# Optimization experiments

Measured on AMD Instinct MI355X. Metric: run time of the kernel, lower is better.

## Reference

```python
import jax, jax.numpy as jnp
import numpy as np

N = 100000
E = 1600000
HID = 128
NODE_DIM = 128


def _sage_conv(h, src, dst, W_l, b_l, W_r, n_nodes):
    # PyG SAGEConv (mean aggr): out = lin_l(mean_{j in N(i)} h_j) + lin_r(h_i)
    msg = h[src]                                            # [E, d] gather
    s = jax.ops.segment_sum(msg, dst, num_segments=n_nodes)  # [N, d]
    cnt = jax.ops.segment_sum(jnp.ones((msg.shape[0], 1), h.dtype), dst,
                              num_segments=n_nodes)          # [N, 1]
    agg = jnp.where(cnt > 0, s / jnp.maximum(cnt, 1.0), 0.0)
    return agg @ W_l + b_l + h @ W_r


def setup_inputs() -> dict:
    key = jax.random.key(0)
    ks = jax.random.split(key, 12)
    sc = 0.05
    return {
        "pos": jax.random.normal(ks[0], (N, 3), jnp.float32),
        "atomic_number": jax.random.randint(ks[1], (N,), 0, 10, jnp.int64)
            if jax.config.jax_enable_x64 else jax.random.randint(ks[1], (N,), 0, 10, jnp.int32),
        "edge_index": jax.random.randint(ks[2], (2, E), 0, N, jnp.int32),
        # input_proj: Linear(4, HID) — stored as [in, out]
        "W_in": jax.random.normal(ks[3], (4, HID), jnp.float32) * sc,
        "b_in": jnp.zeros((HID,), jnp.float32),
        # conv1: SAGEConv(HID, HID): lin_l (bias), lin_r (no bias)
        "W1_l": jax.random.normal(ks[4], (HID, HID), jnp.float32) * sc,
        "b1": jnp.zeros((HID,), jnp.float32),
        "W1_r": jax.random.normal(ks[5], (HID, HID), jnp.float32) * sc,
        # conv2
        "W2_l": jax.random.normal(ks[6], (HID, HID), jnp.float32) * sc,
        "b2": jnp.zeros((HID,), jnp.float32),
        "W2_r": jax.random.normal(ks[7], (HID, HID), jnp.float32) * sc,
        # out: Linear(HID, NODE_DIM)
        "W_out": jax.random.normal(ks[8], (HID, NODE_DIM), jnp.float32) * sc,
        "b_out": jnp.zeros((NODE_DIM,), jnp.float32),
    }


def reference(pos, atomic_number, edge_index, W_in, b_in, W1_l, b1, W1_r,
              W2_l, b2, W2_r, W_out, b_out):
    src, dst = edge_index[0], edge_index[1]
    z_atom = (atomic_number.astype(pos.dtype) / 10.0)[:, None]   # [N, 1]
    x = jnp.concatenate([z_atom, pos], axis=-1)                   # [N, 4]
    h = jax.nn.relu(x @ W_in + b_in)
    h = jax.nn.relu(_sage_conv(h, src, dst, W1_l, b1, W1_r, h.shape[0]))
    h = jax.nn.relu(_sage_conv(h, src, dst, W2_l, b2, W2_r, h.shape[0]))
    node_states = h @ W_out + b_out                               # [N, node_dim]
    return node_states.mean(axis=0), node_states
```

## Files before the change

### kernel.cpp

```cpp
#include <hip/hip_runtime.h>

#define HID 128
#define BK_SHIFT 9
#define BK_NODES 512
#define EDGES_PER_BLKA 8192

typedef _Float16 half_t;
typedef __attribute__((ext_vector_type(8))) _Float16 half8;
typedef __attribute__((ext_vector_type(4))) _Float16 half4;
typedef __attribute__((ext_vector_type(2))) _Float16 half2_t;
typedef __attribute__((ext_vector_type(4))) float f32x4;

__global__ __launch_bounds__(256) void k_init(int* __restrict__ bkcnt,
                                              float* __restrict__ outmean) {
  int i = threadIdx.x;
  bkcnt[i] = 0;
  if (i < HID) outmean[i] = 0.f;
}

__global__ __launch_bounds__(256) void k_packW(const float* __restrict__ W,
                                               half_t* __restrict__ out) {
  int tid = blockIdx.x * 256 + threadIdx.x;
  int lane = tid & 63;
  int frag = tid >> 6;
  int ks = frag >> 3, nt = frag & 7;
  int k0 = ks * 32 + ((lane >> 4) << 3);
  int col = nt * 16 + (lane & 15);
  half8 v;
#pragma unroll
  for (int i = 0; i < 8; ++i) v[i] = (half_t)W[(k0 + i) * HID + col];
  *(half8*)&out[(size_t)tid * 8] = v;
}

__global__ __launch_bounds__(256) void k_embed(const float* __restrict__ pos,
                                               const int* __restrict__ an,
                                               const float* __restrict__ Win,
                                               const float* __restrict__ bin,
                                               half_t* __restrict__ h, int n) {
  int t = blockIdx.x * 256 + threadIdx.x;
  int i = t >> 5, cg = t & 31;
  if (i >= n) return;
  int j0 = cg << 2;
  float z  = (float)an[i] / 10.0f;
  float px = pos[3 * i + 0], py = pos[3 * i + 1], pz = pos[3 * i + 2];
  float4 w0 = *(const float4*)&Win[0 * HID + j0];
  float4 w1 = *(const float4*)&Win[1 * HID + j0];
  float4 w2 = *(const float4*)&Win[2 * HID + j0];
  float4 w3 = *(const float4*)&Win[3 * HID + j0];
  float4 b  = *(const float4*)&bin[j0];
  float4 o;
  o.x = fmaxf(fmaf(z, w0.x, fmaf(px, w1.x, fmaf(py, w2.x, fmaf(pz, w3.x, b.x)))), 0.f);
  o.y = fmaxf(fmaf(z, w0.y, fmaf(px, w1.y, fmaf(py, w2.y, fmaf(pz, w3.y, b.y)))), 0.f);
  o.z = fmaxf(fmaf(z, w0.z, fmaf(px, w1.z, fmaf(py, w2.z, fmaf(pz, w3.z, b.z)))), 0.f);
  o.w = fmaxf(fmaf(z, w0.w, fmaf(px, w1.w, fmaf(py, w2.w, fmaf(pz, w3.w, b.w)))), 0.f);
  half4 ph;
  ph.x = (half_t)o.x; ph.y = (half_t)o.y; ph.z = (half_t)o.z; ph.w = (half_t)o.w;
  *(half4*)&h[(size_t)i * HID + j0] = ph;
}

__global__ __launch_bounds__(1024) void k_bhist(const int* __restrict__ dst,
                                                int* __restrict__ bkcnt, int e) {
  __shared__ int hist[256];
  int t = threadIdx.x;
  if (t < 256) hist[t] = 0;
  __syncthreads();
  int e0 = blockIdx.x * EDGES_PER_BLKA;
#pragma unroll
  for (int i = 0; i < 8; ++i) {
    int idx = e0 + i * 1024 + t;
    if (idx < e) atomicAdd(&hist[dst[idx] >> BK_SHIFT], 1);
  }
  __syncthreads();
  if (t < 256 && hist[t] > 0) atomicAdd(&bkcnt[t], hist[t]);
}

__global__ __launch_bounds__(256) void k_bscan(const int* __restrict__ bkcnt,
                                               int* __restrict__ bkbase,
                                               int* __restrict__ bcur,
                                               int nbuck, int e) {
  __shared__ int buf[256];
  int t = threadIdx.x;
  int v = (t < nbuck) ? bkcnt[t] : 0;
  buf[t] = v;
  __syncthreads();
  for (int d = 1; d < 256; d <<= 1) {
    int u = (t >= d) ? buf[t - d] : 0;
    __syncthreads();
    buf[t] += u;
    __syncthreads();
  }
  int excl = buf[t] - v;
  if (t < nbuck) { bkbase[t] = excl; bcur[t] = excl; }
  if (t == 0) bkbase[nbuck] = e;
}

__global__ __launch_bounds__(1024) void k_bucketA(const int* __restrict__ src,
                                                  const int* __restrict__ dst,
                                                  int* __restrict__ bcur,
                                                  unsigned* __restrict__ ebuf,
                                                  int e, int nbuck) {
  __shared__ unsigned stage[EDGES_PER_BLKA];
  __shared__ unsigned char stagebk[EDGES_PER_BLKA];
  __shared__ int hist[256];
  __shared__ int base[256];
  __shared__ int resv[256];
  int t = threadIdx.x;
  if (t < 256) hist[t] = 0;
  __syncthreads();

  int e0 = blockIdx.x * EDGES_PER_BLKA;
  int myb[8], myr[8];
  unsigned mypk[8];
#pragma unroll
  for (int i = 0; i < 8; ++i) {
    int idx = e0 + i * 1024 + t;
    if (idx < e) {
      int d = dst[idx];
      int s = src[idx];
      int b = d >> BK_SHIFT;
      myb[i] = b;
      myr[i] = atomicAdd(&hist[b], 1);
      mypk[i] = ((unsigned)s << BK_SHIFT) | (unsigned)(d & (BK_NODES - 1));
    } else {
      myb[i] = -1;
    }
  }
  __syncthreads();
  if (t < 256) base[t] = hist[t];
  __syncthreads();
  for (int d = 1; d < 256; d <<= 1) {
    int v = 0;
    if (t < 256 && t >= d) v = base[t - d];
    __syncthreads();
    if (t < 256 && t >= d) base[t] += v;
    __syncthreads();
  }
  if (t < 256) {
    base[t] -= hist[t];
    resv[t] = (t < nbuck && hist[t] > 0) ? atomicAdd(&bcur[t], hist[t]) : 0;
  }
  __syncthreads();
#pragma unroll
  for (int i = 0; i < 8; ++i) {
    if (myb[i] >= 0) {
      int slot = base[myb[i]] + myr[i];
      stage[slot] = mypk[i];
      stagebk[slot] = (unsigned char)myb[i];
    }
  }
  __syncthreads();
  int total = e - e0;
  if (total > EDGES_PER_BLKA) total = EDGES_PER_BLKA;
  for (int s = t; s < total; s += 1024) {
    int b = stagebk[s];
    ebuf[resv[b] + (s - base[b])] = stage[s];
  }
}

__global__ __launch_bounds__(256) void k_bucketB(const unsigned* __restrict__ ebuf,
                                                 const int* __restrict__ bkbase,
                                                 int* __restrict__ offs,
                                                 int* __restrict__ csr, int n, int e) {
  __shared__ int hist[BK_NODES];
  __shared__ int pscan[256];
  int b = blockIdx.x;
  int n0 = b << BK_SHIFT;
  int t = threadIdx.x;
  int ebeg = bkbase[b], eend = bkbase[b + 1];
  hist[t] = 0; hist[t + 256] = 0;
  __syncthreads();
  for (int idx = ebeg + t; idx < eend; idx += 256) {
    atomicAdd(&hist[ebuf[idx] & (BK_NODES - 1)], 1);
  }
  __syncthreads();
  int h0 = hist[2 * t], h1 = hist[2 * t + 1];
  int ps = h0 + h1;
  pscan[t] = ps;
  __syncthreads();
  for (int d = 1; d < 256; d <<= 1) {
    int u = (t >= d) ? pscan[t - d] : 0;
    __syncthreads();
    pscan[t] += u;
    __syncthreads();
  }
  int base0 = ebeg + (pscan[t] - ps);
  int g0 = n0 + 2 * t, g1 = g0 + 1;
  if (g0 < n) offs[g0] = base0;
  if (g1 < n) offs[g1] = base0 + h0;
  __syncthreads();
  hist[2 * t] = base0;
  hist[2 * t + 1] = base0 + h0;
  __syncthreads();
  for (int idx = ebeg + t; idx < eend; idx += 256) {
    unsigned pk = ebuf[idx];
    int dl = pk & (BK_NODES - 1);
    int s = (int)(pk >> BK_SHIFT);
    int slot = atomicAdd(&hist[dl], 1);
    csr[slot] = s;
  }
  if (b == 0 && t == 0) offs[n] = e;
}

__global__ __launch_bounds__(256) void k_aggmean_f16(const half_t* __restrict__ h,
                                                     const int* __restrict__ csr,
                                                     const int* __restrict__ offs,
                                                     half_t* __restrict__ out, int n) {
  int w = (blockIdx.x * 256 + threadIdx.x) >> 6;
  int lane = threadIdx.x & 63;
  if (w >= n) return;
  int cs = lane & 15, es = lane >> 4;
  int beg = offs[w], end = offs[w + 1];
  size_t coff = (size_t)(cs * 8);
  float acc[8];
#pragma unroll
  for (int j = 0; j < 8; ++j) acc[j] = 0.f;
  int e = beg;
  for (; e + 16 <= end; e += 16) {
    int s0 = csr[e + es];
    int s1 = csr[e + 4 + es];
    int s2 = csr[e + 8 + es];
    int s3 = csr[e + 12 + es];
    half8 v0 = *(const half8*)&h[(size_t)s0 * HID + coff];
    half8 v1 = *(const half8*)&h[(size_t)s1 * HID + coff];
    half8 v2 = *(const half8*)&h[(size_t)s2 * HID + coff];
    half8 v3 = *(const half8*)&h[(size_t)s3 * HID + coff];
#pragma unroll
    for (int j = 0; j < 8; ++j)
      acc[j] += ((float)v0[j] + (float)v1[j]) + ((float)v2[j] + (float)v3[j]);
  }
  for (; e < end; e += 4) {
    int ee = e + es;
    if (ee < end) {
      int s = csr[ee];
      half8 v = *(const half8*)&h[(size_t)s * HID + coff];
#pragma unroll
      for (int j = 0; j < 8; ++j) acc[j] += (float)v[j];
    }
  }
#pragma unroll
  for (int j = 0; j < 8; ++j) {
    acc[j] += __shfl_xor(acc[j], 16, 64);
    acc[j] += __shfl_xor(acc[j], 32, 64);
  }
  if (es == 0) {
    int c = end - beg;
    float inv = (c > 0) ? 1.0f / (float)c : 0.0f;
    half8 o;
#pragma unroll
    for (int j = 0; j < 8; ++j) o[j] = (half_t)(acc[j] * inv);
    *(half8*)&out[(size_t)w * HID + coff] = o;
  }
}

__global__ __launch_bounds__(256) void k_sage_mfma(const half_t* __restrict__ ha,
                                                   const half_t* __restrict__ hs,
                                                   const half_t* __restrict__ wl,
                                                   const half_t* __restrict__ wr,
                                                   const float* __restrict__ bias,
                                                   half_t* __restrict__ out, int n) {
  int lane = threadIdx.x & 63;
  int wid = threadIdx.x >> 6;
  int row0 = blockIdx.x * 64 + wid * 16;
  if (row0 >= n) return;
  int arow = row0 + (lane & 15);
  int arowc = arow < n ? arow : n - 1;
  size_t abase = (size_t)arowc * HID + ((lane >> 4) << 3);
  const half8* WL = (const half8*)wl;
  const half8* WR = (const half8*)wr;
  f32x4 acc[8];
#pragma unroll
  for (int t = 0; t < 8; ++t) acc[t] = (f32x4){0.f, 0.f, 0.f, 0.f};
#pragma unroll
  for (int ks = 0; ks < 4; ++ks) {
    half8 aD = *(const half8*)&ha[abase + ks * 32];
    half8 aH = *(const half8*)&hs[abase + ks * 32];
    int fb = ks * 8;
#pragma unroll
    for (int nt = 0; nt < 8; ++nt) {
      half8 bl = WL[(size_t)(fb + nt) * 64 + lane];
      half8 br = WR[(size_t)(fb + nt) * 64 + lane];
      acc[nt] = __builtin_amdgcn_mfma_f32_16x16x32_f16(aD, bl, acc[nt], 0, 0, 0);
      acc[nt] = __builtin_amdgcn_mfma_f32_16x16x32_f16(aH, br, acc[nt], 0, 0, 0);
    }
  }
  int rbase = row0 + ((lane >> 4) << 2);
  int cl = lane & 15;
#pragma unroll
  for (int nt = 0; nt < 8; ++nt) {
    int col = nt * 16 + cl;
    float bv = bias[col];
#pragma unroll
    for (int r = 0; r < 4; ++r) {
      int row = rbase + r;
      if (row < n) {
        float v = fmaxf(acc[nt][r] + bv, 0.f);
        out[(size_t)row * HID + col] = (half_t)v;
      }
    }
  }
}

__global__ __launch_bounds__(256) void k_single_mfma(const half_t* __restrict__ hs,
                                                     const half_t* __restrict__ w,
                                                     const float* __restrict__ bias,
                                                     float* __restrict__ out,
                                                     float* __restrict__ part, int n) {
  __shared__ float colsum[HID];
  int tid = threadIdx.x;
  int lane = tid & 63;
  int wid = tid >> 6;
  if (tid < HID) colsum[tid] = 0.f;
  __syncthreads();
  int row0 = blockIdx.x * 64 + wid * 16;
  bool active = row0 < n;
  f32x4 acc[8];
#pragma unroll
  for (int t = 0; t < 8; ++t) acc[t] = (f32x4){0.f, 0.f, 0.f, 0.f};
  if (active) {
    int arow = row0 + (lane & 15);
    int arowc = arow < n ? arow : n - 1;
    size_t abase = (size_t)arowc * HID + ((lane >> 4) << 3);
    const half8* W8 = (const half8*)w;
#pragma unroll
    for (int ks = 0; ks < 4; ++ks) {
      half8 aH = *(const half8*)&hs[abase + ks * 32];
      int fb = ks * 8;
#pragma unroll
      for (int nt = 0; nt < 8; ++nt) {
        half8 b = W8[(size_t)(fb + nt) * 64 + lane];
        acc[nt] = __builtin_amdgcn_mfma_f32_16x16x32_f16(aH, b, acc[nt], 0, 0, 0);
      }
    }
    int rbase = row0 + ((lane >> 4) << 2);
    int cl = lane & 15;
#pragma unroll
    for (int nt = 0; nt < 8; ++nt) {
      int col = nt * 16 + cl;
      float bv = bias[col];
      float csum = 0.f;
#pragma unroll
      for (int r = 0; r < 4; ++r) {
        int row = rbase + r;
        if (row < n) {
          float v = acc[nt][r] + bv;
          out[(size_t)row * HID + col] = v;
          csum += v;
        }
      }
      atomicAdd(&colsum[col], csum);
    }
  }
  __syncthreads();
  if (tid < HID) part[(size_t)blockIdx.x * HID + tid] = colsum[tid];
}

__global__ __launch_bounds__(256) void k_colfinal(const float* __restrict__ part,
                                                  float* __restrict__ outmean,
                                                  int rows, float inv) {
  __shared__ float red[256];
  int t = threadIdx.x;
  int col = t & 127, half = t >> 7;
  int r0 = blockIdx.x * 256;
  float s = 0.f;
  for (int r = half; r < 256; r += 2) {
    int row = r0 + r;
    if (row < rows) s += part[(size_t)row * HID + col];
  }
  red[t] = s;
  __syncthreads();
  if (t < 128) atomicAdd(&outmean[col], (red[t] + red[t + 128]) * inv);
}

extern "C" void kernel_launch(void* const* d_in, const int* in_sizes, int n_in,
                              void* d_out, int out_size, void* d_ws, size_t ws_size,
                              hipStream_t stream) {
  const float* pos  = (const float*)d_in[0];
  const int*   an   = (const int*)d_in[1];
  const int*   ei   = (const int*)d_in[2];
  const float* Win  = (const float*)d_in[3];
  const float* bin  = (const float*)d_in[4];
  const float* W1l  = (const float*)d_in[5];
  const float* b1   = (const float*)d_in[6];
  const float* W1r  = (const float*)d_in[7];
  const float* W2l  = (const float*)d_in[8];
  const float* b2   = (const float*)d_in[9];
  const float* W2r  = (const float*)d_in[10];
  const float* Wout = (const float*)d_in[11];
  const float* bout = (const float*)d_in[12];

  int N = in_sizes[0] / 3;
  int E = in_sizes[2] / 2;
  const int* srcl = ei;
  const int* dstl = ei + E;

  float* outmean = (float*)d_out;
  float* ns      = (float*)d_out + HID;

  char* p = (char*)d_ws;
  auto take = [&](size_t bytes) {
    char* q = p;
    p += (bytes + 255) & ~(size_t)255;
    return q;
  };
  half_t*   H0      = (half_t*)take((size_t)N * HID * 2);
  half_t*   H1      = (half_t*)take((size_t)N * HID * 2);
  half_t*   H2      = (half_t*)take((size_t)N * HID * 2);
  half_t*   D       = (half_t*)take((size_t)N * HID * 2);
  int*      offs    = (int*)take((size_t)(N + 1) * 4);
  int*      csr     = (int*)take((size_t)E * 4);
  unsigned* ebuf    = (unsigned*)take((size_t)E * 4);
  int*      bkcnt   = (int*)take((size_t)256 * 4);
  int*      bkbase  = (int*)take((size_t)257 * 4);
  int*      bcur    = (int*)take((size_t)256 * 4);
  half_t*   pW1l    = (half_t*)take((size_t)16384 * 2);
  half_t*   pW1r    = (half_t*)take((size_t)16384 * 2);
  half_t*   pW2l    = (half_t*)take((size_t)16384 * 2);
  half_t*   pW2r    = (half_t*)take((size_t)16384 * 2);
  half_t*   pWout   = (half_t*)take((size_t)16384 * 2);
  int gSage = (N + 63) / 64;
  float*    colpart = (float*)take((size_t)gSage * HID * 4);

  int nbuck  = (N + BK_NODES - 1) / BK_NODES;
  int gEmbed = (int)(((size_t)N * 32 + 255) / 256);
  int gWave  = (N + 3) / 4;
  int gBktA  = (E + EDGES_PER_BLKA - 1) / EDGES_PER_BLKA;

  k_init<<<1, 256, 0, stream>>>(bkcnt, outmean);
  k_packW<<<8, 256, 0, stream>>>(W1l, pW1l);
  k_packW<<<8, 256, 0, stream>>>(W1r, pW1r);
  k_packW<<<8, 256, 0, stream>>>(W2l, pW2l);
  k_packW<<<8, 256, 0, stream>>>(W2r, pW2r);
  k_packW<<<8, 256, 0, stream>>>(Wout, pWout);
  k_embed<<<gEmbed, 256, 0, stream>>>(pos, an, Win, bin, H0, N);
  k_bhist<<<gBktA, 1024, 0, stream>>>(dstl, bkcnt, E);
  k_bscan<<<1, 256, 0, stream>>>(bkcnt, bkbase, bcur, nbuck, E);
  k_bucketA<<<gBktA, 1024, 0, stream>>>(srcl, dstl, bcur, ebuf, E, nbuck);
  k_bucketB<<<nbuck, 256, 0, stream>>>(ebuf, bkbase, offs, csr, N, E);

  k_aggmean_f16<<<gWave, 256, 0, stream>>>(H0, csr, offs, D, N);
  k_sage_mfma<<<gSage, 256, 0, stream>>>(D, H0, pW1l, pW1r, b1, H1, N);
  k_aggmean_f16<<<gWave, 256, 0, stream>>>(H1, csr, offs, D, N);
  k_sage_mfma<<<gSage, 256, 0, stream>>>(D, H1, pW2l, pW2r, b2, H2, N);
  k_single_mfma<<<gSage, 256, 0, stream>>>(H2, pWout, bout, ns, colpart, N);
  k_colfinal<<<(gSage + 255) / 256, 256, 0, stream>>>(colpart, outmean, gSage, 1.0f / (float)N);
}
```

Before: 320.8 us.

## Use fixed-capacity edge buckets to drop histogram and scan passes

Each destination bucket gets a fixed slot range of BKCAP entries, so the separate bucket-histogram and scan kernels disappear. Bucket cursors are initialised to i*BKCAP, and each node's CSR range now comes from separate begin and end offset arrays. The bucketing kernel also drops its LDS staging and scan, writing edges straight to global memory, and the five weight-packing launches are merged into one. In exchange, global writes are less coalesced, and nothing checks whether a bucket overflows BKCAP, so heavily skewed degree distributions would corrupt memory.

```diff
diff --git a/kernel.cpp b/kernel.cpp
--- a/kernel.cpp
+++ b/kernel.cpp
@@ -3,24 +3,35 @@
 #define HID 128
 #define BK_SHIFT 9
 #define BK_NODES 512
+#define BKCAP 10240
 #define EDGES_PER_BLKA 8192
 
 typedef _Float16 half_t;
 typedef __attribute__((ext_vector_type(8))) _Float16 half8;
 typedef __attribute__((ext_vector_type(4))) _Float16 half4;
-typedef __attribute__((ext_vector_type(2))) _Float16 half2_t;
 typedef __attribute__((ext_vector_type(4))) float f32x4;
 
-__global__ __launch_bounds__(256) void k_init(int* __restrict__ bkcnt,
+__global__ __launch_bounds__(256) void k_init(int* __restrict__ bcur,
                                               float* __restrict__ outmean) {
   int i = threadIdx.x;
-  bkcnt[i] = 0;
+  bcur[i] = i * BKCAP;
   if (i < HID) outmean[i] = 0.f;
 }
 
-__global__ __launch_bounds__(256) void k_packW(const float* __restrict__ W,
-                                               half_t* __restrict__ out) {
-  int tid = blockIdx.x * 256 + threadIdx.x;
+__global__ __launch_bounds__(256) void k_packW5(const float* __restrict__ w0,
+                                                const float* __restrict__ w1,
+                                                const float* __restrict__ w2,
+                                                const float* __restrict__ w3,
+                                                const float* __restrict__ w4,
+                                                half_t* __restrict__ o0,
+                                                half_t* __restrict__ o1,
+                                                half_t* __restrict__ o2,
+                                                half_t* __restrict__ o3,
+                                                half_t* __restrict__ o4) {
+  int m = blockIdx.x >> 3;
+  const float* W = (m == 0) ? w0 : (m == 1) ? w1 : (m == 2) ? w2 : (m == 3) ? w3 : w4;
+  half_t* out = (m == 0) ? o0 : (m == 1) ? o1 : (m == 2) ? o2 : (m == 3) ? o3 : o4;
+  int tid = (blockIdx.x & 7) * 256 + threadIdx.x;
   int lane = tid & 63;
   int frag = tid >> 6;
   int ks = frag >> 3, nt = frag & 7;
@@ -58,56 +69,16 @@
   *(half4*)&h[(size_t)i * HID + j0] = ph;
 }
 
-__global__ __launch_bounds__(1024) void k_bhist(const int* __restrict__ dst,
-                                                int* __restrict__ bkcnt, int e) {
-  __shared__ int hist[256];
-  int t = threadIdx.x;
-  if (t < 256) hist[t] = 0;
-  __syncthreads();
-  int e0 = blockIdx.x * EDGES_PER_BLKA;
-#pragma unroll
-  for (int i = 0; i < 8; ++i) {
-    int idx = e0 + i * 1024 + t;
-    if (idx < e) atomicAdd(&hist[dst[idx] >> BK_SHIFT], 1);
-  }
-  __syncthreads();
-  if (t < 256 && hist[t] > 0) atomicAdd(&bkcnt[t], hist[t]);
-}
-
-__global__ __launch_bounds__(256) void k_bscan(const int* __restrict__ bkcnt,
-                                               int* __restrict__ bkbase,
-                                               int* __restrict__ bcur,
-                                               int nbuck, int e) {
-  __shared__ int buf[256];
-  int t = threadIdx.x;
-  int v = (t < nbuck) ? bkcnt[t] : 0;
-  buf[t] = v;
-  __syncthreads();
-  for (int d = 1; d < 256; d <<= 1) {
-    int u = (t >= d) ? buf[t - d] : 0;
-    __syncthreads();
-    buf[t] += u;
-    __syncthreads();
-  }
-  int excl = buf[t] - v;
-  if (t < nbuck) { bkbase[t] = excl; bcur[t] = excl; }
-  if (t == 0) bkbase[nbuck] = e;
-}
-
 __global__ __launch_bounds__(1024) void k_bucketA(const int* __restrict__ src,
                                                   const int* __restrict__ dst,
                                                   int* __restrict__ bcur,
                                                   unsigned* __restrict__ ebuf,
-                                                  int e, int nbuck) {
-  __shared__ unsigned stage[EDGES_PER_BLKA];
-  __shared__ unsigned char stagebk[EDGES_PER_BLKA];
+                                                  int e) {
   __shared__ int hist[256];
-  __shared__ int base[256];
   __shared__ int resv[256];
   int t = threadIdx.x;
   if (t < 256) hist[t] = 0;
   __syncthreads();
-
   int e0 = blockIdx.x * EDGES_PER_BLKA;
   int myb[8], myr[8];
   unsigned mypk[8];
@@ -126,47 +97,25 @@
     }
   }
   __syncthreads();
-  if (t < 256) base[t] = hist[t];
-  __syncthreads();
-  for (int d = 1; d < 256; d <<= 1) {
-    int v = 0;
-    if (t < 256 && t >= d) v = base[t - d];
-    __syncthreads();
-    if (t < 256 && t >= d) base[t] += v;
-    __syncthreads();
-  }
-  if (t < 256) {
-    base[t] -= hist[t];
-    resv[t] = (t < nbuck && hist[t] > 0) ? atomicAdd(&bcur[t], hist[t]) : 0;
-  }
+  if (t < 256) resv[t] = (hist[t] > 0) ? atomicAdd(&bcur[t], hist[t]) : 0;
   __syncthreads();
 #pragma unroll
   for (int i = 0; i < 8; ++i) {
-    if (myb[i] >= 0) {
-      int slot = base[myb[i]] + myr[i];
-      stage[slot] = mypk[i];
-      stagebk[slot] = (unsigned char)myb[i];
-    }
-  }
-  __syncthreads();
-  int total = e - e0;
-  if (total > EDGES_PER_BLKA) total = EDGES_PER_BLKA;
-  for (int s = t; s < total; s += 1024) {
-    int b = stagebk[s];
-    ebuf[resv[b] + (s - base[b])] = stage[s];
+    if (myb[i] >= 0) ebuf[resv[myb[i]] + myr[i]] = mypk[i];
   }
 }
 
 __global__ __launch_bounds__(256) void k_bucketB(const unsigned* __restrict__ ebuf,
-                                                 const int* __restrict__ bkbase,
+                                                 const int* __restrict__ bkend,
                                                  int* __restrict__ offs,
-                                                 int* __restrict__ csr, int n, int e) {
+                                                 int* __restrict__ offsE,
+                                                 int* __restrict__ csr, int n) {
   __shared__ int hist[BK_NODES];
   __shared__ int pscan[256];
   int b = blockIdx.x;
   int n0 = b << BK_SHIFT;
   int t = threadIdx.x;
-  int ebeg = bkbase[b], eend = bkbase[b + 1];
+  int ebeg = b * BKCAP, eend = bkend[b];
   hist[t] = 0; hist[t + 256] = 0;
   __syncthreads();
   for (int idx = ebeg + t; idx < eend; idx += 256) {
@@ -185,8 +134,8 @@
   }
   int base0 = ebeg + (pscan[t] - ps);
   int g0 = n0 + 2 * t, g1 = g0 + 1;
-  if (g0 < n) offs[g0] = base0;
-  if (g1 < n) offs[g1] = base0 + h0;
+  if (g0 < n) { offs[g0] = base0;      offsE[g0] = base0 + h0; }
+  if (g1 < n) { offs[g1] = base0 + h0; offsE[g1] = base0 + h0 + h1; }
   __syncthreads();
   hist[2 * t] = base0;
   hist[2 * t + 1] = base0 + h0;
@@ -194,22 +143,21 @@
   for (int idx = ebeg + t; idx < eend; idx += 256) {
     unsigned pk = ebuf[idx];
     int dl = pk & (BK_NODES - 1);
-    int s = (int)(pk >> BK_SHIFT);
     int slot = atomicAdd(&hist[dl], 1);
-    csr[slot] = s;
-  }
-  if (b == 0 && t == 0) offs[n] = e;
+    csr[slot] = (int)(pk >> BK_SHIFT);
+  }
 }
 
 __global__ __launch_bounds__(256) void k_aggmean_f16(const half_t* __restrict__ h,
                                                      const int* __restrict__ csr,
                                                      const int* __restrict__ offs,
+                                                     const int* __restrict__ offsE,
                                                      half_t* __restrict__ out, int n) {
   int w = (blockIdx.x * 256 + threadIdx.x) >> 6;
   int lane = threadIdx.x & 63;
   if (w >= n) return;
   int cs = lane & 15, es = lane >> 4;
-  int beg = offs[w], end = offs[w + 1];
+  int beg = offs[w], end = offsE[w];
   size_t coff = (size_t)(cs * 8);
   float acc[8];
 #pragma unroll
@@ -402,15 +350,15 @@
     p += (bytes + 255) & ~(size_t)255;
     return q;
   };
+  int nbuck = (N + BK_NODES - 1) / BK_NODES;
   half_t*   H0      = (half_t*)take((size_t)N * HID * 2);
   half_t*   H1      = (half_t*)take((size_t)N * HID * 2);
   half_t*   H2      = (half_t*)take((size_t)N * HID * 2);
   half_t*   D       = (half_t*)take((size_t)N * HID * 2);
-  int*      offs    = (int*)take((size_t)(N + 1) * 4);
-  int*      csr     = (int*)take((size_t)E * 4);
-  unsigned* ebuf    = (unsigned*)take((size_t)E * 4);
-  int*      bkcnt   = (int*)take((size_t)256 * 4);
-  int*      bkbase  = (int*)take((size_t)257 * 4);
+  int*      offs    = (int*)take((size_t)N * 4);
+  int*      offsE   = (int*)take((size_t)N * 4);
+  int*      csr     = (int*)take((size_t)nbuck * BKCAP * 4);
+  unsigned* ebuf    = (unsigned*)take((size_t)nbuck * BKCAP * 4);
   int*      bcur    = (int*)take((size_t)256 * 4);
   half_t*   pW1l    = (half_t*)take((size_t)16384 * 2);
   half_t*   pW1r    = (half_t*)take((size_t)16384 * 2);
@@ -420,26 +368,20 @@
   int gSage = (N + 63) / 64;
   float*    colpart = (float*)take((size_t)gSage * HID * 4);
 
-  int nbuck  = (N + BK_NODES - 1) / BK_NODES;
   int gEmbed = (int)(((size_t)N * 32 + 255) / 256);
   int gWave  = (N + 3) / 4;
   int gBktA  = (E + EDGES_PER_BLKA - 1) / EDGES_PER_BLKA;
 
-  k_init<<<1, 256, 0, stream>>>(bkcnt, outmean);
-  k_packW<<<8, 256, 0, stream>>>(W1l, pW1l);
-  k_packW<<<8, 256, 0, stream>>>(W1r, pW1r);
-  k_packW<<<8, 256, 0, stream>>>(W2l, pW2l);
-  k_packW<<<8, 256, 0, stream>>>(W2r, pW2r);
-  k_packW<<<8, 256, 0, stream>>>(Wout, pWout);
+  k_init<<<1, 256, 0, stream>>>(bcur, outmean);
+  k_packW5<<<40, 256, 0, stream>>>(W1l, W1r, W2l, W2r, Wout,
+                                   pW1l, pW1r, pW2l, pW2r, pWout);
   k_embed<<<gEmbed, 256, 0, stream>>>(pos, an, Win, bin, H0, N);
-  k_bhist<<<gBktA, 1024, 0, stream>>>(dstl, bkcnt, E);
-  k_bscan<<<1, 256, 0, stream>>>(bkcnt, bkbase, bcur, nbuck, E);
-  k_bucketA<<<gBktA, 1024, 0, stream>>>(srcl, dstl, bcur, ebuf, E, nbuck);
-  k_bucketB<<<nbuck, 256, 0, stream>>>(ebuf, bkbase, offs, csr, N, E);
-
-  k_aggmean_f16<<<gWave, 256, 0, stream>>>(H0, csr, offs, D, N);
+  k_bucketA<<<gBktA, 1024, 0, stream>>>(srcl, dstl, bcur, ebuf, E);
+  k_bucketB<<<nbuck, 256, 0, stream>>>(ebuf, bcur, offs, offsE, csr, N);
+
+  k_aggmean_f16<<<gWave, 256, 0, stream>>>(H0, csr, offs, offsE, D, N);
   k_sage_mfma<<<gSage, 256, 0, stream>>>(D, H0, pW1l, pW1r, b1, H1, N);
-  k_aggmean_f16<<<gWave, 256, 0, stream>>>(H1, csr, offs, D, N);
+  k_aggmean_f16<<<gWave, 256, 0, stream>>>(H1, csr, offs, offsE, D, N);
   k_sage_mfma<<<gSage, 256, 0, stream>>>(D, H1, pW2l, pW2r, b2, H2, N);
   k_single_mfma<<<gSage, 256, 0, stream>>>(H2, pWout, bout, ns, colpart, N);
   k_colfinal<<<(gSage + 255) / 256, 256, 0, stream>>>(colpart, outmean, gSage, 1.0f / (float)N);
```

Result: faster. 309.3 us (-3.6%).
